# Kernel optimization log

Measured on AMD Instinct MI355X. Metric: run time of the kernel, lower is better.

The kernel has to match this reference:

```python
import jax, jax.numpy as jnp
import numpy as np
from jax import lax

B, C_IN, C_OUT, K, N_W, L = 32, 256, 256, 7, 8, 4096
SQ = C_IN // 32  # squeezed dim = 8
STRIDE, PAD = 1, 3


def setup_inputs() -> dict:
    key = jax.random.key(0)
    ks = jax.random.split(key, 8)
    s = 0.05
    return {
        "x": jax.random.normal(ks[0], (B, C_IN, L), dtype=jnp.float32),
        "conv_weight": jax.random.normal(ks[1], (C_OUT, C_IN, K, N_W), dtype=jnp.float32) * s,
        "w1": jax.random.normal(ks[2], (C_IN, SQ), dtype=jnp.float32) * s,   # linear1 weight (x @ w1)
        "b1": jax.random.normal(ks[3], (SQ,), dtype=jnp.float32) * s,
        "wk": jax.random.normal(ks[4], (SQ, K), dtype=jnp.float32) * s,      # kernel head
        "wi": jax.random.normal(ks[5], (SQ, C_IN), dtype=jnp.float32) * s,   # inc head
        "wo": jax.random.normal(ks[6], (SQ, C_OUT), dtype=jnp.float32) * s,  # outc head
        "wn": jax.random.normal(ks[7], (SQ, N_W), dtype=jnp.float32) * s,    # nums head
    }


def reference(x, conv_weight, w1, b1, wk, wi, wo, wn):
    # SqueezeFeedForward: AdaptiveAvgPool1d(1) == mean over length, then Linear + exact GELU
    pooled = jnp.mean(x, axis=-1)                        # [B, C_in]
    h = jax.nn.gelu(pooled @ w1 + b1, approximate=False)  # [B, SQ]

    kr = jax.nn.sigmoid(h @ wk)          # [B, K]
    inc = jax.nn.sigmoid(h @ wi)         # [B, C_in]
    outc = jax.nn.sigmoid(h @ wo)        # [B, C_out]
    nums = jax.nn.softmax(h @ wn, -1)    # [B, N_w]

    # Per-sample mixed weights: sum over num_weight of 4-way outer-product gated base weight
    w = jnp.einsum('bk,bi,bo,bn,oikn->boik', kr, inc, outc, nums, conv_weight)  # [B,O,I,K]

    b, o, i, k = w.shape
    l = x.shape[-1]
    # Batched per-sample conv via grouped conv: groups = B
    lhs = x.reshape(1, b * i, l)         # [1, B*I, L]
    rhs = w.reshape(b * o, i, k)         # [B*O, I, K]
    out = lax.conv_general_dilated(
        lhs, rhs,
        window_strides=(STRIDE,),
        padding=[(PAD, PAD)],
        dimension_numbers=('NCH', 'OIH', 'NCH'),
        feature_group_count=b,
    )
    return out.reshape(b, o, -1)         # [B, O, L_out]
```

## Files before the change

### kernel.cpp

```cpp
#include <hip/hip_runtime.h>
#include <hip/hip_bf16.h>
#include <math.h>

#define B_   32
#define CI   256
#define CO   256
#define KW   7
#define NW   8
#define SQD  8
#define L_   4096

typedef __attribute__((ext_vector_type(8))) __bf16 bf16x8;
typedef __attribute__((ext_vector_type(4))) __bf16 bf16x4;
typedef __attribute__((ext_vector_type(4))) float  f32x4;

static __device__ __forceinline__ unsigned short f2bf(float f) {
    unsigned int u = __builtin_bit_cast(unsigned int, f);
    u += 0x7FFFu + ((u >> 16) & 1u);
    return (unsigned short)(u >> 16);
}
static __device__ __forceinline__ uint2 pack4bf(float a, float b, float c, float d) {
    bf16x4 v;
    v[0] = (__bf16)a; v[1] = (__bf16)b; v[2] = (__bf16)c; v[3] = (__bf16)d;
    return __builtin_bit_cast(uint2, v);
}

__global__ __launch_bounds__(256) void k1_mean(
        const float* __restrict__ x, float* __restrict__ pooled) {
    int row = blockIdx.x;
    const float* p = x + (size_t)row * L_;
    int t = threadIdx.x;
    float s = 0.f;
#pragma unroll
    for (int it = 0; it < 4; ++it) {
        float4 v = *(const float4*)(p + (size_t)(t + 256 * it) * 4);
        s += v.x + v.y + v.z + v.w;
    }
    for (int m = 1; m <= 32; m <<= 1) s += __shfl_xor(s, m);
    __shared__ float wsum[4];
    if ((t & 63) == 0) wsum[t >> 6] = s;
    __syncthreads();
    if (t == 0)
        pooled[row] = (wsum[0] + wsum[1] + wsum[2] + wsum[3]) * (1.0f / L_);
}

__global__ __launch_bounds__(64) void k2_gates(
        const float* __restrict__ pooled,
        const float* __restrict__ w1, const float* __restrict__ b1,
        const float* __restrict__ wk, const float* __restrict__ wi,
        const float* __restrict__ wo, const float* __restrict__ wn,
        float* __restrict__ kr, float* __restrict__ inc,
        float* __restrict__ outc, float* __restrict__ nums)
{
    int b = blockIdx.x, lane = threadIdx.x;
    float pc[4];
#pragma unroll
    for (int j = 0; j < 4; ++j)
        pc[j] = pooled[b * CI + lane + 64 * j];
    float h[SQD];
#pragma unroll
    for (int s = 0; s < SQD; ++s) {
        float ps = 0.f;
#pragma unroll
        for (int j = 0; j < 4; ++j)
            ps += pc[j] * w1[(lane + 64 * j) * SQD + s];
        for (int m = 1; m <= 32; m <<= 1) ps += __shfl_xor(ps, m);
        float z = ps + b1[s];
        h[s] = 0.5f * z * (1.0f + erff(z * 0.70710678118654752f));
    }
    if (lane < KW) {
        float a = 0.f;
#pragma unroll
        for (int s = 0; s < SQD; ++s) a += h[s] * wk[s * KW + lane];
        kr[b * 8 + lane] = 1.0f / (1.0f + expf(-a));
    }
    if (lane < NW) {
        float e[NW]; float mx = -1e30f;
#pragma unroll
        for (int n = 0; n < NW; ++n) {
            float a = 0.f;
#pragma unroll
            for (int s = 0; s < SQD; ++s) a += h[s] * wn[s * NW + n];
            e[n] = a; mx = fmaxf(mx, a);
        }
        float den = 0.f;
#pragma unroll
        for (int n = 0; n < NW; ++n) den += expf(e[n] - mx);
        nums[b * NW + lane] = expf(e[lane] - mx) / den;
    }
#pragma unroll
    for (int j = 0; j < 4; ++j) {
        int c = lane + 64 * j;
        float a = 0.f, o2 = 0.f;
#pragma unroll
        for (int s = 0; s < SQD; ++s) {
            a  += h[s] * wi[s * CI + c];
            o2 += h[s] * wo[s * CO + c];
        }
        inc[b * CI + c]  = 1.0f / (1.0f + expf(-a));
        outc[b * CO + c] = 1.0f / (1.0f + expf(-o2));
    }
}

__global__ __launch_bounds__(256) void k3_wgen(
        const float* __restrict__ cw,
        const float* __restrict__ kr, const float* __restrict__ inc,
        const float* __restrict__ outc, const float* __restrict__ nums,
        unsigned short* __restrict__ W2) {
    __shared__ float s_nums[B_][NW];
    __shared__ float s_kr[B_][KW];
    __shared__ float s_inc[B_][32];
    __shared__ float s_outc[B_][8];
    int t = threadIdx.x;
    int ic = blockIdx.x & 7, o0 = (blockIdx.x >> 3) * 8;
    s_nums[t >> 3][t & 7] = nums[t];
    if (t < B_ * KW) s_kr[t / KW][t % KW] = kr[(t / KW) * 8 + (t % KW)];
    for (int u = t; u < 32 * 32; u += 256) {
        int bb = u >> 5, ii = u & 31;
        s_inc[bb][ii] = inc[bb * CI + ic * 32 + ii];
    }
    for (int u = t; u < 32 * 8; u += 256) {
        int bb = u >> 3, oo = u & 7;
        s_outc[bb][oo] = outc[bb * CO + o0 + oo];
    }
    __syncthreads();
    int ii = t & 31, oo = t >> 5;
    int o = o0 + oo, i = ic * 32 + ii;
    float cwv[KW][NW];
    const float* p = cw + ((size_t)(o * CI + i)) * (KW * NW);
#pragma unroll
    for (int k = 0; k < KW; ++k)
#pragma unroll
        for (int n = 0; n < NW; ++n) cwv[k][n] = p[k * NW + n];
    for (int bb = 0; bb < B_; ++bb) {
        float gio = s_inc[bb][ii] * s_outc[bb][oo];
#pragma unroll
        for (int k = 0; k < KW; ++k) {
            float sk = 0.f;
#pragma unroll
            for (int n = 0; n < NW; ++n) sk += s_nums[bb][n] * cwv[k][n];
            float w = s_kr[bb][k] * gio * sk;
            W2[(((size_t)(bb * KW + k) * 8 + ic) * CO + o) * 32 + ii] = f2bf(w);
        }
    }
}

__global__ __launch_bounds__(512, 2) void k4_conv(
        const float* __restrict__ x,
        const unsigned short* __restrict__ W2,
        float* __restrict__ out) {
    __shared__ __align__(16) unsigned short xs[262 * 256];
    int bid = blockIdx.x;
    int wg  = (bid & 7) * 64 + (bid >> 3);
    int b = wg >> 4, l0 = (wg & 15) * 256;
    int t = threadIdx.x;
    const float* xb = x + (size_t)b * CI * L_;

    {
        int ch = (t & 31) + 32 * (t >> 8);
        int g  = (t >> 5) & 7;
#pragma unroll
        for (int it = 0; it < 8; ++it) {
            int i0 = g * 4 + it * 32;
            float4 f0 = *(const float4*)(xb + (size_t)(i0 + 0) * L_ + l0 + ch * 4);
            float4 f1 = *(const float4*)(xb + (size_t)(i0 + 1) * L_ + l0 + ch * 4);
            float4 f2 = *(const float4*)(xb + (size_t)(i0 + 2) * L_ + l0 + ch * 4);
            float4 f3 = *(const float4*)(xb + (size_t)(i0 + 3) * L_ + l0 + ch * 4);
            int u = i0 >> 3, h = (i0 >> 2) & 1;
#pragma unroll
            for (int j = 0; j < 4; ++j) {
                int r = 4 * ch + j + 3;
                uint2 w = pack4bf((&f0.x)[j], (&f1.x)[j], (&f2.x)[j], (&f3.x)[j]);
                int sw = (r & 7) ^ ((r >> 2) & 7);
                *(uint2*)(xs + r * 256 + ((u ^ sw) * 8) + h * 4) = w;
            }
        }
    }
    if (t < 128) {
        bool left = t < 64;
        int tt = left ? t : t - 64;
        int i0 = tt * 4;
        int gl4 = left ? l0 - 4 : l0 + 256;
        bool ok = left ? (l0 > 0) : (l0 + 256 < L_);
        float4 f[4];
#pragma unroll
        for (int d = 0; d < 4; ++d)
            f[d] = ok ? *(const float4*)(xb + (size_t)(i0 + d) * L_ + gl4)
                      : make_float4(0.f, 0.f, 0.f, 0.f);
        int u = i0 >> 3, h = (i0 >> 2) & 1;
#pragma unroll
        for (int j = 0; j < 4; ++j) {
            if (left && j == 0) continue;
            if (!left && j == 3) continue;
            int r = left ? (j - 1) : (259 + j);
            uint2 w = pack4bf((&f[0].x)[j], (&f[1].x)[j], (&f[2].x)[j], (&f[3].x)[j]);
            int sw = (r & 7) ^ ((r >> 2) & 7);
            *(uint2*)(xs + r * 256 + ((u ^ sw) * 8) + h * 4) = w;
        }
    }
    __syncthreads();

    int lane = t & 63, wid = t >> 6;
    int o_base = (wid & 1) * 128;
    int l_off  = (wid >> 1) * 64;
    int ml = lane & 15, kg = lane >> 4;

    f32x4 acc[8][4];
#pragma unroll
    for (int a = 0; a < 8; ++a)
#pragma unroll
        for (int c = 0; c < 4; ++c) acc[a][c] = (f32x4){0.f, 0.f, 0.f, 0.f};

    const unsigned short* wbase = W2 + (size_t)b * (56 * CO * 32);

    auto LOADF = [&](bf16x8 (&AF)[8], bf16x8 (&BF)[4], int S) {
        int k_ = S >> 3, icc_ = S & 7;
        const unsigned short* wkc = wbase + (size_t)S * (CO * 32);
#pragma unroll
        for (int mt = 0; mt < 8; ++mt)
            AF[mt] = *(const bf16x8*)(wkc + (o_base + mt * 16 + ml) * 32 + kg * 8);
#pragma unroll
        for (int nt = 0; nt < 4; ++nt) {
            int r = l_off + nt * 16 + ml + k_;
            int unit = (icc_ * 4 + kg) ^ ((r & 7) ^ ((r >> 2) & 7));
            BF[nt] = *(const bf16x8*)(xs + r * 256 + unit * 8);
        }
    };
    auto DOMFMA = [&](bf16x8 (&AF)[8], bf16x8 (&BF)[4]) {
        __builtin_amdgcn_s_setprio(1);
#pragma unroll
        for (int mt = 0; mt < 8; ++mt)
#pragma unroll
            for (int nt = 0; nt < 4; ++nt)
                acc[mt][nt] = __builtin_amdgcn_mfma_f32_16x16x32_bf16(
                    AF[mt], BF[nt], acc[mt][nt], 0, 0, 0);
        __builtin_amdgcn_s_setprio(0);
    };

    bf16x8 afA[8], bfA[4], afB[8], bfB[4];
    LOADF(afA, bfA, 0);
    for (int s = 0; s < 56; s += 2) {
        LOADF(afB, bfB, s + 1);
        DOMFMA(afA, bfA);
        if (s + 2 < 56) LOADF(afA, bfA, s + 2);
        DOMFMA(afB, bfB);
    }

#pragma unroll
    for (int mt = 0; mt < 8; ++mt) {
        int o = o_base + mt * 16 + kg * 4;
#pragma unroll
        for (int nt = 0; nt < 4; ++nt) {
            int l = l0 + l_off + nt * 16 + ml;
            float* po = out + ((size_t)(b * CO + o)) * L_ + l;
#pragma unroll
            for (int q = 0; q < 4; ++q)
                po[(size_t)q * L_] = acc[mt][nt][q];
        }
    }
}

extern "C" void kernel_launch(void* const* d_in, const int* in_sizes, int n_in,
                              void* d_out, int out_size, void* d_ws, size_t ws_size,
                              hipStream_t stream) {
    const float* x  = (const float*)d_in[0];
    const float* cw = (const float*)d_in[1];
    const float* w1 = (const float*)d_in[2];
    const float* b1 = (const float*)d_in[3];
    const float* wk = (const float*)d_in[4];
    const float* wi = (const float*)d_in[5];
    const float* wo = (const float*)d_in[6];
    const float* wn = (const float*)d_in[7];
    float* out = (float*)d_out;

    char* ws = (char*)d_ws;
    unsigned short* W2 = (unsigned short*)(ws + 0);
    float* pooled = (float*)(ws + 29360128);
    float* kr     = (float*)(ws + 29392896);
    float* inc    = (float*)(ws + 29393920);
    float* outc   = (float*)(ws + 29426688);
    float* nums   = (float*)(ws + 29459456);

    k1_mean<<<B_ * CI, 256, 0, stream>>>(x, pooled);
    k2_gates<<<B_, 64, 0, stream>>>(pooled, w1, b1, wk, wi, wo, wn,
                                    kr, inc, outc, nums);
    k3_wgen<<<256, 256, 0, stream>>>(cw, kr, inc, outc, nums, W2);
    k4_conv<<<512, 512, 0, stream>>>(x, W2, out);
}
```

Before: 192.9 us.

## Use 1024-thread conv blocks with 64x64 wave tiles and padded LDS layout

```diff
diff --git a/kernel.cpp b/kernel.cpp
--- a/kernel.cpp
+++ b/kernel.cpp
@@ -145,11 +145,11 @@
     }
 }
 
-__global__ __launch_bounds__(512, 2) void k4_conv(
+__global__ __launch_bounds__(1024) void k4_conv(
         const float* __restrict__ x,
         const unsigned short* __restrict__ W2,
         float* __restrict__ out) {
-    __shared__ __align__(16) unsigned short xs[262 * 256];
+    __shared__ __align__(16) unsigned short xs[262 * 264];
     int bid = blockIdx.x;
     int wg  = (bid & 7) * 64 + (bid >> 3);
     int b = wg >> 4, l0 = (wg & 15) * 256;
@@ -157,22 +157,24 @@
     const float* xb = x + (size_t)b * CI * L_;
 
     {
-        int ch = (t & 31) + 32 * (t >> 8);
-        int g  = (t >> 5) & 7;
-#pragma unroll
-        for (int it = 0; it < 8; ++it) {
-            int i0 = g * 4 + it * 32;
-            float4 f0 = *(const float4*)(xb + (size_t)(i0 + 0) * L_ + l0 + ch * 4);
-            float4 f1 = *(const float4*)(xb + (size_t)(i0 + 1) * L_ + l0 + ch * 4);
-            float4 f2 = *(const float4*)(xb + (size_t)(i0 + 2) * L_ + l0 + ch * 4);
-            float4 f3 = *(const float4*)(xb + (size_t)(i0 + 3) * L_ + l0 + ch * 4);
-            int u = i0 >> 3, h = (i0 >> 2) & 1;
+        int P = t >> 4, lam = t & 15;
+        int up = P & 31, half = P >> 5;
+        int i0 = (up & 7) * 32 + (up >> 3) * 8;
+#pragma unroll
+        for (int it = 0; it < 2; ++it) {
+            int ch = lam + 16 * (half * 2 + it);
+            const float* src = xb + (size_t)i0 * L_ + l0 + ch * 4;
+            float4 f[8];
+#pragma unroll
+            for (int e = 0; e < 8; ++e)
+                f[e] = *(const float4*)(src + (size_t)e * L_);
 #pragma unroll
             for (int j = 0; j < 4; ++j) {
                 int r = 4 * ch + j + 3;
-                uint2 w = pack4bf((&f0.x)[j], (&f1.x)[j], (&f2.x)[j], (&f3.x)[j]);
-                int sw = (r & 7) ^ ((r >> 2) & 7);
-                *(uint2*)(xs + r * 256 + ((u ^ sw) * 8) + h * 4) = w;
+                uint2 a = pack4bf((&f[0].x)[j], (&f[1].x)[j], (&f[2].x)[j], (&f[3].x)[j]);
+                uint2 c = pack4bf((&f[4].x)[j], (&f[5].x)[j], (&f[6].x)[j], (&f[7].x)[j]);
+                uint4 w; w.x = a.x; w.y = a.y; w.z = c.x; w.w = c.y;
+                *(uint4*)(xs + r * 264 + up * 8) = w;
             }
         }
     }
@@ -187,71 +189,61 @@
         for (int d = 0; d < 4; ++d)
             f[d] = ok ? *(const float4*)(xb + (size_t)(i0 + d) * L_ + gl4)
                       : make_float4(0.f, 0.f, 0.f, 0.f);
-        int u = i0 >> 3, h = (i0 >> 2) & 1;
+        int eo = ((tt >> 1) & 3) * 64 + (tt >> 3) * 8 + (tt & 1) * 4;
 #pragma unroll
         for (int j = 0; j < 4; ++j) {
             if (left && j == 0) continue;
             if (!left && j == 3) continue;
             int r = left ? (j - 1) : (259 + j);
             uint2 w = pack4bf((&f[0].x)[j], (&f[1].x)[j], (&f[2].x)[j], (&f[3].x)[j]);
-            int sw = (r & 7) ^ ((r >> 2) & 7);
-            *(uint2*)(xs + r * 256 + ((u ^ sw) * 8) + h * 4) = w;
+            *(uint2*)(xs + r * 264 + eo) = w;
         }
     }
     __syncthreads();
 
     int lane = t & 63, wid = t >> 6;
-    int o_base = (wid & 1) * 128;
-    int l_off  = (wid >> 1) * 64;
+    int o_base = (wid & 3) * 64;
+    int l_wave = (wid >> 2) * 64;
     int ml = lane & 15, kg = lane >> 4;
 
-    f32x4 acc[8][4];
-#pragma unroll
-    for (int a = 0; a < 8; ++a)
+    f32x4 acc[4][4];
+#pragma unroll
+    for (int a = 0; a < 4; ++a)
 #pragma unroll
         for (int c = 0; c < 4; ++c) acc[a][c] = (f32x4){0.f, 0.f, 0.f, 0.f};
 
-    const unsigned short* wbase = W2 + (size_t)b * (56 * CO * 32);
-
-    auto LOADF = [&](bf16x8 (&AF)[8], bf16x8 (&BF)[4], int S) {
-        int k_ = S >> 3, icc_ = S & 7;
-        const unsigned short* wkc = wbase + (size_t)S * (CO * 32);
-#pragma unroll
-        for (int mt = 0; mt < 8; ++mt)
-            AF[mt] = *(const bf16x8*)(wkc + (o_base + mt * 16 + ml) * 32 + kg * 8);
+    const unsigned short* wA = W2 + (size_t)b * (56 * CO * 32)
+                               + (o_base + ml) * 32 + kg * 8;
+    const unsigned short* xB = xs + (l_wave + ml) * 264 + kg * 64;
+
+    for (int k = 0; k < KW; ++k) {
+#pragma unroll
+        for (int icc = 0; icc < 8; ++icc) {
+            int S = k * 8 + icc;
+            bf16x8 AF[4], BF[4];
+#pragma unroll
+            for (int mt = 0; mt < 4; ++mt)
+                AF[mt] = *(const bf16x8*)(wA + (size_t)S * (CO * 32) + mt * 16 * 32);
+#pragma unroll
+            for (int nt = 0; nt < 4; ++nt)
+                BF[nt] = *(const bf16x8*)(xB + (nt * 16 + k) * 264 + icc * 8);
+            __builtin_amdgcn_s_setprio(1);
+#pragma unroll
+            for (int mt = 0; mt < 4; ++mt)
+#pragma unroll
+                for (int nt = 0; nt < 4; ++nt)
+                    acc[mt][nt] = __builtin_amdgcn_mfma_f32_16x16x32_bf16(
+                        AF[mt], BF[nt], acc[mt][nt], 0, 0, 0);
+            __builtin_amdgcn_s_setprio(0);
+        }
+    }
+
+#pragma unroll
+    for (int mt = 0; mt < 4; ++mt) {
+        int o = o_base + mt * 16 + kg * 4;
 #pragma unroll
         for (int nt = 0; nt < 4; ++nt) {
-            int r = l_off + nt * 16 + ml + k_;
-            int unit = (icc_ * 4 + kg) ^ ((r & 7) ^ ((r >> 2) & 7));
-            BF[nt] = *(const bf16x8*)(xs + r * 256 + unit * 8);
-        }
-    };
-    auto DOMFMA = [&](bf16x8 (&AF)[8], bf16x8 (&BF)[4]) {
-        __builtin_amdgcn_s_setprio(1);
-#pragma unroll
-        for (int mt = 0; mt < 8; ++mt)
-#pragma unroll
-            for (int nt = 0; nt < 4; ++nt)
-                acc[mt][nt] = __builtin_amdgcn_mfma_f32_16x16x32_bf16(
-                    AF[mt], BF[nt], acc[mt][nt], 0, 0, 0);
-        __builtin_amdgcn_s_setprio(0);
-    };
-
-    bf16x8 afA[8], bfA[4], afB[8], bfB[4];
-    LOADF(afA, bfA, 0);
-    for (int s = 0; s < 56; s += 2) {
-        LOADF(afB, bfB, s + 1);
-        DOMFMA(afA, bfA);
-        if (s + 2 < 56) LOADF(afA, bfA, s + 2);
-        DOMFMA(afB, bfB);
-    }
-
-#pragma unroll
-    for (int mt = 0; mt < 8; ++mt) {
-        int o = o_base + mt * 16 + kg * 4;
-#pragma unroll
-        for (int nt = 0; nt < 4; ++nt) {
-            int l = l0 + l_off + nt * 16 + ml;
+            int l = l0 + l_wave + nt * 16 + ml;
             float* po = out + ((size_t)(b * CO + o)) * L_ + l;
 #pragma unroll
             for (int q = 0; q < 4; ++q)
@@ -285,5 +277,5 @@
     k2_gates<<<B_, 64, 0, stream>>>(pooled, w1, b1, wk, wi, wo, wn,
                                     kr, inc, outc, nums);
     k3_wgen<<<256, 256, 0, stream>>>(cw, kr, inc, outc, nums, W2);
-    k4_conv<<<512, 512, 0, stream>>>(x, W2, out);
-}
+    k4_conv<<<512, 1024, 0, stream>>>(x, W2, out);
+}
```

Measured after the change: 192.2 us. Within noise of the previous version (-0.4%).
